# Optimization experiments

Measured on AMD Instinct MI355X. Metric: run time of the kernel, lower is better.

The kernel has to match this reference:

```python
import math
import jax, jax.numpy as jnp
import numpy as np

B = 4096
IN_FEATURES = 512
OUT_FEATURES = 1024
SPARSITY = 0.01  # kwta.sparsity
X_DENSITY = 0.1  # fraction of active bits in the binary SDR input


def setup_inputs() -> dict:
    key = jax.random.key(0)
    kx, kw = jax.random.split(key)
    # binary sparse SDR input (the module counts nonzeros, expects sparse binary x)
    x = (jax.random.uniform(kx, (B, IN_FEATURES)) < X_DENSITY).astype(jnp.float32)
    weight = jax.random.normal(kw, (OUT_FEATURES, IN_FEATURES), dtype=jnp.float32)
    return {"x": x, "weight": weight}


def reference(x, weight):
    Bn, in_f = x.shape
    out_f = weight.shape[0]
    k_active = math.ceil(SPARSITY * out_f)   # serial MP steps (11)
    k_in = math.ceil(SPARSITY * in_f)        # kwta winners on xr (6)
    rows = jnp.arange(Bn)

    nonzero = jnp.sum(x != 0, axis=1)
    lambd = (3 * jnp.max(nonzero) * in_f).astype(jnp.float32)

    def wta(r):  # one-hot argmax per row -> binary [B, out_f]
        idx = jnp.argmax(r, axis=1)
        return jnp.zeros_like(r).at[rows, idx].set(1.0)

    def kwta(v):  # binary top-k per row -> binary [B, in_f]
        _, idx = jax.lax.top_k(v, k_in)
        return jnp.zeros_like(v).at[rows[:, None], idx].set(1.0)

    two_x = 2.0 * x
    wT = weight.T  # [in_f, out_f]

    def step(carry, _):
        encoded, xr = carry
        residual = (two_x - xr) @ wT - lambd * encoded      # [B, out_f]
        encoded = encoded + wta(residual)
        xr = kwta(encoded @ weight)                          # [B, in_f]
        return (encoded, xr), None

    init = (jnp.zeros((Bn, out_f), jnp.float32), jnp.zeros_like(x))
    (encoded, xr), _ = jax.lax.scan(step, init, None, length=k_active)
    return encoded, xr
```

## Files before the change

kernel.cpp:

```cpp
#include <hip/hip_runtime.h>

#define IN_F 512
#define OUT_F 1024
#define K_ACTIVE 11
#define K_IN 6

__global__ __launch_bounds__(256) void transpose_w_kernel(const float* __restrict__ w,
                                                          float* __restrict__ wT) {
    __shared__ float tile[32][33];
    const int tx = threadIdx.x & 31;
    const int ty = threadIdx.x >> 5;
    const int i0 = blockIdx.x * 32;
    const int j0 = blockIdx.y * 32;
#pragma unroll
    for (int k = 0; k < 4; ++k)
        tile[ty + 8 * k][tx] = w[(size_t)(j0 + ty + 8 * k) * IN_F + (i0 + tx)];
    __syncthreads();
#pragma unroll
    for (int k = 0; k < 4; ++k)
        wT[(size_t)(i0 + ty + 8 * k) * OUT_F + (j0 + tx)] = tile[tx][ty + 8 * k];
}
__global__ void zero_row_f_kernel(float* __restrict__ wT) {
    wT[(size_t)IN_F * OUT_F + blockIdx.x * 256 + threadIdx.x] = 0.0f;
}

__device__ __forceinline__ unsigned long long pack_key(double v, unsigned rev,
                                                       unsigned long long mask) {
    unsigned long long b = (unsigned long long)__double_as_longlong(v);
    unsigned long long m =
        (unsigned long long)((long long)b >> 63) | 0x8000000000000000ull;
    unsigned long long u = b ^ m;
    return (u & ~mask) | (unsigned long long)rev;
}

__device__ __forceinline__ unsigned hi_key(double v) {
    const int hi = __double2hiint(v);
    return (unsigned)hi ^ ((unsigned)(hi >> 31) | 0x80000000u);
}

template <int C>
__device__ __forceinline__ unsigned maxdpp(unsigned v) {
    unsigned t = (unsigned)__builtin_amdgcn_update_dpp(0, (int)v, C, 0xF, 0xF, true);
    return t > v ? t : v;
}
__device__ __forceinline__ unsigned wave_umax(unsigned v) {
    v = maxdpp<0x111>(v);
    v = maxdpp<0x112>(v);
    v = maxdpp<0x114>(v);
    v = maxdpp<0x118>(v);
    v = maxdpp<0x142>(v);
    v = maxdpp<0x143>(v);
    return (unsigned)__builtin_amdgcn_readlane((int)v, 63);
}

__device__ __forceinline__ unsigned long long wave_max_key(unsigned long long k) {
    const unsigned h = (unsigned)(k >> 32), l = (unsigned)k;
    const unsigned gh = wave_umax(h);
    const unsigned long long tied = __ballot(h == gh);
    unsigned gl;
    if (__popcll(tied) == 1) {
        gl = (unsigned)__builtin_amdgcn_readlane((int)l,
                                                 (int)__ffsll((long long)tied) - 1);
    } else {
        gl = wave_umax((h == gh) ? l : 0u);
    }
    return ((unsigned long long)gh << 32) | gl;
}

__device__ __forceinline__ void half_add0(double* rh, const float* __restrict__ w,
                                          int i, int lane, int wv) {
#pragma unroll
    for (int s = 0; s < 8; ++s) {
        const int j = (wv << 9) | ((s >> 2) << 8) | (lane << 2) | (s & 3);
        rh[s] += (double)w[(size_t)j * IN_F + i];
    }
}
__device__ __forceinline__ void half_axpy0(double* rh, const float* __restrict__ w,
                                           int i, double sgn, int lane, int wv) {
#pragma unroll
    for (int s = 0; s < 8; ++s) {
        const int j = (wv << 9) | ((s >> 2) << 8) | (lane << 2) | (s & 3);
        rh[s] += sgn * (double)w[(size_t)j * IN_F + i];
    }
}

template <int MODE>
__global__ __launch_bounds__(128) void bmp_kernel(const float* __restrict__ x,
                                                  const float* __restrict__ w,
                                                  const float* __restrict__ wT,
                                                  float* __restrict__ out, int rows) {
    __shared__ unsigned short act[IN_F + 8];
    __shared__ unsigned gu32[2][2];
    __shared__ int gjw[2][2];
    __shared__ unsigned long long kx[2];
    __shared__ int axlist[16];
    __shared__ int axn;
    const int lane = threadIdx.x & 63;
    const int wv = threadIdx.x >> 6;
    const int row = blockIdx.x;
    if (row >= rows) return;

    const float* xrow = x + (size_t)row * IN_F;
    int cnt = 0;
#pragma unroll
    for (int c = 0; c < IN_F / 64; ++c) {
        bool pbit = xrow[c * 64 + lane] != 0.0f;
        unsigned long long m = __ballot(pbit);
        int pre = __popcll(m & ((1ull << lane) - 1ull));
        if (wv == 0 && pbit) act[cnt + pre] = (unsigned short)(c * 64 + lane);
        cnt += __popcll(m);
    }
    if (wv == 0 && lane < 2) act[cnt + lane] = (unsigned short)IN_F;
    __syncthreads();

    double r[8];
#pragma unroll
    for (int s = 0; s < 8; ++s) r[s] = 0.0;
    if constexpr (MODE == 1) {
        const int base = (wv << 9) + (lane << 2);
        const float* pa = wT + ((size_t)act[0] << 10) + base;
        const float* pb = wT + ((size_t)act[1] << 10) + base;
        float4 c0 = *(const float4*)pa, c1 = *(const float4*)(pa + 256);
        float4 c2 = *(const float4*)pb, c3 = *(const float4*)(pb + 256);
#pragma unroll 1
        for (int k = 0; k < cnt; k += 2) {
            float4 n0 = c0, n1 = c1, n2 = c2, n3 = c3;
            if (k + 2 < cnt) {
                const float* qa = wT + ((size_t)act[k + 2] << 10) + base;
                const float* qb = wT + ((size_t)act[k + 3] << 10) + base;
                n0 = *(const float4*)qa;  n1 = *(const float4*)(qa + 256);
                n2 = *(const float4*)qb;  n3 = *(const float4*)(qb + 256);
            }
            r[0] += (double)c0.x + (double)c2.x;  r[1] += (double)c0.y + (double)c2.y;
            r[2] += (double)c0.z + (double)c2.z;  r[3] += (double)c0.w + (double)c2.w;
            r[4] += (double)c1.x + (double)c3.x;  r[5] += (double)c1.y + (double)c3.y;
            r[6] += (double)c1.z + (double)c3.z;  r[7] += (double)c1.w + (double)c3.w;
            c0 = n0; c1 = n1; c2 = n2; c3 = n3;
        }
    } else {
#pragma unroll 1
        for (int k = 0; k < cnt; ++k) half_add0(r, w, act[k], lane, wv);
    }
#pragma unroll
    for (int s = 0; s < 8; ++s) r[s] *= 2.0;

    double vd[8];
#pragma unroll
    for (int p = 0; p < 8; ++p) vd[p] = 0.0;

    unsigned enc = 0;
    unsigned selmask = 0;
    int O0 = -1, O1 = -1, O2 = -1, O3 = -1, O4 = -1, O5 = -1;

#pragma unroll 1
    for (int t = 0; t < K_ACTIVE; ++t) {
        unsigned k8[8];
#pragma unroll
        for (int s = 0; s < 8; ++s) {
            const unsigned key = hi_key(r[s]);
            k8[s] = (enc & (1u << s)) ? 0u : key;
        }
        {
            unsigned lm = k8[0];
#pragma unroll
            for (int s = 1; s < 8; ++s) lm = k8[s] > lm ? k8[s] : lm;
            const unsigned g = wave_umax(lm);
            const unsigned long long tied = __ballot(lm == g);
            unsigned mm = 0;
#pragma unroll
            for (int s = 0; s < 8; ++s) mm |= (k8[s] == g) ? (1u << s) : 0u;
            const int L = (int)__ffsll((long long)tied) - 1;
            const unsigned mmL = (unsigned)__builtin_amdgcn_readlane((int)mm, L);
            int jw;
            if (__builtin_expect((__popcll(tied) == 1) && !(mmL & (mmL - 1)), 1)) {
                const int bi = __ffs(mmL) - 1;
                jw = (wv << 9) | ((bi >> 2) << 8) | (L << 2) | (bi & 3);
            } else {
                unsigned long long kb = 0;
#pragma unroll
                for (int s = 0; s < 8; ++s) {
                    const int j = (wv << 9) | ((s >> 2) << 8) | (lane << 2) | (s & 3);
                    const unsigned long long fk =
                        pack_key(r[s], 1023u ^ (unsigned)j, 1023ull);
                    kb = (k8[s] == g && fk > kb) ? fk : kb;
                }
                const unsigned long long gk = wave_max_key(kb);
                jw = 1023 ^ (int)(gk & 1023ull);
            }
            if (lane == 0) {
                gu32[t & 1][wv] = g;
                gjw[t & 1][wv] = jw;
            }
        }
        __syncthreads();
        const unsigned ga = gu32[t & 1][0], gb = gu32[t & 1][1];
        int bestj;
        if (__builtin_expect(ga != gb, 1)) {
            bestj = (gb > ga) ? gjw[t & 1][1] : gjw[t & 1][0];
        } else {
            unsigned long long kb = 0;
#pragma unroll
            for (int s = 0; s < 8; ++s) {
                const int j = (wv << 9) | ((s >> 2) << 8) | (lane << 2) | (s & 3);
                const unsigned long long fk =
                    pack_key(r[s], 1023u ^ (unsigned)j, 1023ull);
                kb = (k8[s] == ga && fk > kb) ? fk : kb;
            }
            const unsigned long long wm = wave_max_key(kb);
            if (lane == 0) kx[wv] = wm;
            __syncthreads();
            const unsigned long long A = kx[0], B = kx[1];
            bestj = 1023 ^ (int)((A > B ? A : B) & 1023ull);
        }
        bestj = __builtin_amdgcn_readfirstlane(bestj);
        if ((bestj >> 9) == wv && ((bestj >> 2) & 63) == lane)
            enc |= 1u << ((((bestj >> 8) & 1) << 2) | (bestj & 3));

        if (wv == 0) {
            const float* wr = w + ((size_t)bestj << 9) + (lane << 2);
            const float4 f0 = *(const float4*)wr;
            const float4 f1 = *(const float4*)(wr + 256);
            vd[0] += (double)f0.x;  vd[1] += (double)f0.y;
            vd[2] += (double)f0.z;  vd[3] += (double)f0.w;
            vd[4] += (double)f1.x;  vd[5] += (double)f1.y;
            vd[6] += (double)f1.z;  vd[7] += (double)f1.w;

            int N[6];
            unsigned kk[8];
#pragma unroll
            for (int p = 0; p < 8; ++p) kk[p] = hi_key(vd[p]);
#pragma unroll
            for (int s2 = 0; s2 < K_IN; ++s2) {
                unsigned lm = kk[0];
#pragma unroll
                for (int p = 1; p < 8; ++p) lm = kk[p] > lm ? kk[p] : lm;
                const unsigned g2 = wave_umax(lm);
                const unsigned long long tied2 = __ballot(lm == g2);
                unsigned mm2 = 0;
#pragma unroll
                for (int p = 0; p < 8; ++p) mm2 |= (kk[p] == g2) ? (1u << p) : 0u;
                const int L2 = (int)__ffsll((long long)tied2) - 1;
                const unsigned mmL2 =
                    (unsigned)__builtin_amdgcn_readlane((int)mm2, L2);
                int n;
                if (__builtin_expect((__popcll(tied2) == 1) && !(mmL2 & (mmL2 - 1)),
                                     1)) {
                    const int bp = __ffs(mmL2) - 1;
                    n = ((bp >> 2) << 8) | (L2 << 2) | (bp & 3);
#pragma unroll
                    for (int p = 0; p < 8; ++p) kk[p] = (kk[p] == g2) ? 0u : kk[p];
                } else {
                    unsigned long long kb = 0;
#pragma unroll
                    for (int p = 0; p < 8; ++p) {
                        const int i = ((p >> 2) << 8) | (lane << 2) | (p & 3);
                        const unsigned long long fk =
                            pack_key(vd[p], 511u ^ (unsigned)i, 511ull);
                        kb = (kk[p] == g2 && fk > kb) ? fk : kb;
                    }
                    const unsigned long long gk = wave_max_key(kb);
                    n = 511 ^ (int)(gk & 511ull);
                    const int ln = (n >> 2) & 63;
                    const int bp = (((n >> 8) & 1) << 2) | (n & 3);
#pragma unroll
                    for (int p = 0; p < 8; ++p)
                        kk[p] = (lane == ln && p == bp) ? 0u : kk[p];
                }
                N[s2] = __builtin_amdgcn_readfirstlane(n);
            }
            if (t == K_ACTIVE - 1) {
                selmask = 0;
#pragma unroll
                for (int p = 0; p < 8; ++p) selmask |= (kk[p] == 0u) ? (1u << p) : 0u;
            }

            if (lane == 0) {
                int n2 = 0;
                if (t == 0) {
#pragma unroll
                    for (int b = 0; b < 6; ++b) axlist[n2++] = ~N[b];
                } else if (t < K_ACTIVE - 1) {
#pragma unroll
                    for (int a2 = 0; a2 < 6; ++a2) {
                        const int o = (a2 == 0) ? O0 : (a2 == 1) ? O1 : (a2 == 2) ? O2
                                      : (a2 == 3) ? O3 : (a2 == 4) ? O4 : O5;
                        const bool stay = (o == N[0]) | (o == N[1]) | (o == N[2]) |
                                          (o == N[3]) | (o == N[4]) | (o == N[5]);
                        if (!stay) axlist[n2++] = o;
                    }
#pragma unroll
                    for (int b = 0; b < 6; ++b) {
                        const int nn = N[b];
                        const bool was = (nn == O0) | (nn == O1) | (nn == O2) |
                                         (nn == O3) | (nn == O4) | (nn == O5);
                        if (!was) axlist[n2++] = ~nn;
                    }
                }
                axn = n2;
            }
            O0 = N[0]; O1 = N[1]; O2 = N[2]; O3 = N[3]; O4 = N[4]; O5 = N[5];
        }
        __syncthreads();

        const int nax = axn;
        if (nax > 0) {
            if constexpr (MODE == 1) {
                const int base = (wv << 9) + (lane << 2);
                int e0 = axlist[0];
                {
                    const int i0 = (e0 < 0) ? ~e0 : e0;
                    const float* p = wT + ((size_t)i0 << 10) + base;
                    float4 A0 = *(const float4*)p;
                    float4 A1 = *(const float4*)(p + 256);
#pragma unroll 1
                    for (int k = 0; k < nax; ++k) {
                        float4 B0 = A0, B1 = A1;
                        int e1 = 0;
                        if (k + 1 < nax) {
                            e1 = axlist[k + 1];
                            const int i1 = (e1 < 0) ? ~e1 : e1;
                            const float* q = wT + ((size_t)i1 << 10) + base;
                            B0 = *(const float4*)q;
                            B1 = *(const float4*)(q + 256);
                        }
                        const double sg = (e0 < 0) ? -1.0 : 1.0;
                        r[0] += sg * (double)A0.x;  r[1] += sg * (double)A0.y;
                        r[2] += sg * (double)A0.z;  r[3] += sg * (double)A0.w;
                        r[4] += sg * (double)A1.x;  r[5] += sg * (double)A1.y;
                        r[6] += sg * (double)A1.z;  r[7] += sg * (double)A1.w;
                        A0 = B0; A1 = B1; e0 = e1;
                    }
                }
            } else {
#pragma unroll 1
                for (int k = 0; k < nax; ++k) {
                    const int e = axlist[k];
                    const int i = (e < 0) ? ~e : e;
                    half_axpy0(r, w, i, (e < 0) ? -1.0 : 1.0, lane, wv);
                }
            }
        }
    }

    float* oe = out + (size_t)row * OUT_F + (wv << 9) + (lane << 2);
#pragma unroll
    for (int c = 0; c < 2; ++c) {
        float4 v;
        v.x = (enc & (1u << (4 * c + 0))) ? 1.0f : 0.0f;
        v.y = (enc & (1u << (4 * c + 1))) ? 1.0f : 0.0f;
        v.z = (enc & (1u << (4 * c + 2))) ? 1.0f : 0.0f;
        v.w = (enc & (1u << (4 * c + 3))) ? 1.0f : 0.0f;
        *(float4*)(oe + (c << 8)) = v;
    }
    if (wv == 0) {
        float* ox = out + (size_t)rows * OUT_F + (size_t)row * IN_F + (lane << 2);
#pragma unroll
        for (int c = 0; c < 2; ++c) {
            float4 v;
            v.x = (selmask & (1u << (4 * c + 0))) ? 1.0f : 0.0f;
            v.y = (selmask & (1u << (4 * c + 1))) ? 1.0f : 0.0f;
            v.z = (selmask & (1u << (4 * c + 2))) ? 1.0f : 0.0f;
            v.w = (selmask & (1u << (4 * c + 3))) ? 1.0f : 0.0f;
            *(float4*)(ox + (c << 8)) = v;
        }
    }
}

extern "C" void kernel_launch(void* const* d_in, const int* in_sizes, int n_in,
                              void* d_out, int out_size, void* d_ws, size_t ws_size,
                              hipStream_t stream) {
    const float* x = (const float*)d_in[0];
    const float* w = (const float*)d_in[1];
    float* out = (float*)d_out;
    const int rows = in_sizes[0] / IN_F;

    const size_t need_f = (size_t)(IN_F + 1) * OUT_F * sizeof(float);

    if (d_ws != nullptr && ws_size >= need_f) {
        float* wT = (float*)d_ws;
        transpose_w_kernel<<<dim3(IN_F / 32, OUT_F / 32), 256, 0, stream>>>(w, wT);
        zero_row_f_kernel<<<OUT_F / 256, 256, 0, stream>>>(wT);
        bmp_kernel<1><<<rows, 128, 0, stream>>>(x, w, wT, out, rows);
    } else {
        bmp_kernel<0><<<rows, 128, 0, stream>>>(x, w, nullptr, out, rows);
    }
}
```

Baseline: 152.3 us.

## Process two rows per block, splitting serial kWTA work across waves

Each 128-thread block now handles two batch rows. Both waves share the argmax column scan for both rows, while each wave runs the serial encoded@W and top-k reconstruction for its own row, so that per-row serial work runs in parallel instead of leaving one wave idle. The aim is to remove idle wave time and halve the number of block-wide syncs per row. The cost is doubled register state (two residual vectors of doubles per thread) under a waves_per_eu hint, which may lower occupancy or cause spills.

```diff
diff --git a/kernel.cpp b/kernel.cpp
--- a/kernel.cpp
+++ b/kernel.cpp
@@ -85,118 +85,114 @@
 }
 
 template <int MODE>
-__global__ __launch_bounds__(128) void bmp_kernel(const float* __restrict__ x,
-                                                  const float* __restrict__ w,
-                                                  const float* __restrict__ wT,
-                                                  float* __restrict__ out, int rows) {
-    __shared__ unsigned short act[IN_F + 8];
+__global__ __attribute__((amdgpu_flat_work_group_size(128, 128),
+                          amdgpu_waves_per_eu(1, 4)))
+void bmp_kernel(const float* __restrict__ x, const float* __restrict__ w,
+                const float* __restrict__ wT, float* __restrict__ out, int rows) {
+    __shared__ unsigned short act[2][IN_F + 8];
+    __shared__ int cntS[2];
     __shared__ unsigned gu32[2][2];
     __shared__ int gjw[2][2];
-    __shared__ unsigned long long kx[2];
-    __shared__ int axlist[16];
-    __shared__ int axn;
+    __shared__ unsigned long long kx[2][2];
+    __shared__ int axlist[2][16];
+    __shared__ int axn[2];
     const int lane = threadIdx.x & 63;
     const int wv = threadIdx.x >> 6;
-    const int row = blockIdx.x;
-    if (row >= rows) return;
-
-    const float* xrow = x + (size_t)row * IN_F;
-    int cnt = 0;
-#pragma unroll
-    for (int c = 0; c < IN_F / 64; ++c) {
-        bool pbit = xrow[c * 64 + lane] != 0.0f;
-        unsigned long long m = __ballot(pbit);
-        int pre = __popcll(m & ((1ull << lane) - 1ull));
-        if (wv == 0 && pbit) act[cnt + pre] = (unsigned short)(c * 64 + lane);
-        cnt += __popcll(m);
-    }
-    if (wv == 0 && lane < 2) act[cnt + lane] = (unsigned short)IN_F;
+    const int rowA = blockIdx.x * 2;
+    if (rowA >= rows) return;
+    int rowB = rowA + 1;
+    if (rowB >= rows) rowB = rowA;
+    const int myrow = wv ? rowB : rowA;
+
+    {
+        const float* xrow = x + (size_t)myrow * IN_F;
+        int cnt = 0;
+#pragma unroll
+        for (int c = 0; c < IN_F / 64; ++c) {
+            bool pbit = xrow[c * 64 + lane] != 0.0f;
+            unsigned long long m = __ballot(pbit);
+            int pre = __popcll(m & ((1ull << lane) - 1ull));
+            if (pbit) act[wv][cnt + pre] = (unsigned short)(c * 64 + lane);
+            cnt += __popcll(m);
+        }
+        if (lane < 2) act[wv][cnt + lane] = (unsigned short)IN_F;
+        if (lane == 0) cntS[wv] = cnt;
+    }
     __syncthreads();
-
-    double r[8];
-#pragma unroll
-    for (int s = 0; s < 8; ++s) r[s] = 0.0;
+    const int cntA = cntS[0], cntB = cntS[1];
+
+    double rA[8], rB[8];
+#pragma unroll
+    for (int s = 0; s < 8; ++s) { rA[s] = 0.0; rB[s] = 0.0; }
+    const int base = (wv << 9) + (lane << 2);
     if constexpr (MODE == 1) {
-        const int base = (wv << 9) + (lane << 2);
-        const float* pa = wT + ((size_t)act[0] << 10) + base;
-        const float* pb = wT + ((size_t)act[1] << 10) + base;
-        float4 c0 = *(const float4*)pa, c1 = *(const float4*)(pa + 256);
-        float4 c2 = *(const float4*)pb, c3 = *(const float4*)(pb + 256);
-#pragma unroll 1
-        for (int k = 0; k < cnt; k += 2) {
-            float4 n0 = c0, n1 = c1, n2 = c2, n3 = c3;
-            if (k + 2 < cnt) {
-                const float* qa = wT + ((size_t)act[k + 2] << 10) + base;
-                const float* qb = wT + ((size_t)act[k + 3] << 10) + base;
-                n0 = *(const float4*)qa;  n1 = *(const float4*)(qa + 256);
-                n2 = *(const float4*)qb;  n3 = *(const float4*)(qb + 256);
-            }
-            r[0] += (double)c0.x + (double)c2.x;  r[1] += (double)c0.y + (double)c2.y;
-            r[2] += (double)c0.z + (double)c2.z;  r[3] += (double)c0.w + (double)c2.w;
-            r[4] += (double)c1.x + (double)c3.x;  r[5] += (double)c1.y + (double)c3.y;
-            r[6] += (double)c1.z + (double)c3.z;  r[7] += (double)c1.w + (double)c3.w;
-            c0 = n0; c1 = n1; c2 = n2; c3 = n3;
+#pragma unroll 1
+        for (int rl = 0; rl < 2; ++rl) {
+            double* r = rl ? rB : rA;
+            const unsigned short* a = act[rl];
+            const int cnt = rl ? cntB : cntA;
+            const float* pa = wT + ((size_t)a[0] << 10) + base;
+            const float* pb = wT + ((size_t)a[1] << 10) + base;
+            float4 c0 = *(const float4*)pa, c1 = *(const float4*)(pa + 256);
+            float4 c2 = *(const float4*)pb, c3 = *(const float4*)(pb + 256);
+#pragma unroll 1
+            for (int k = 0; k < cnt; k += 2) {
+                float4 n0 = c0, n1 = c1, n2 = c2, n3 = c3;
+                if (k + 2 < cnt) {
+                    const float* qa = wT + ((size_t)a[k + 2] << 10) + base;
+                    const float* qb = wT + ((size_t)a[k + 3] << 10) + base;
+                    n0 = *(const float4*)qa;  n1 = *(const float4*)(qa + 256);
+                    n2 = *(const float4*)qb;  n3 = *(const float4*)(qb + 256);
+                }
+                r[0] += (double)c0.x + (double)c2.x;
+                r[1] += (double)c0.y + (double)c2.y;
+                r[2] += (double)c0.z + (double)c2.z;
+                r[3] += (double)c0.w + (double)c2.w;
+                r[4] += (double)c1.x + (double)c3.x;
+                r[5] += (double)c1.y + (double)c3.y;
+                r[6] += (double)c1.z + (double)c3.z;
+                r[7] += (double)c1.w + (double)c3.w;
+                c0 = n0; c1 = n1; c2 = n2; c3 = n3;
+            }
         }
     } else {
 #pragma unroll 1
-        for (int k = 0; k < cnt; ++k) half_add0(r, w, act[k], lane, wv);
-    }
-#pragma unroll
-    for (int s = 0; s < 8; ++s) r[s] *= 2.0;
+        for (int k = 0; k < cntA; ++k) half_add0(rA, w, act[0][k], lane, wv);
+#pragma unroll 1
+        for (int k = 0; k < cntB; ++k) half_add0(rB, w, act[1][k], lane, wv);
+    }
+#pragma unroll
+    for (int s = 0; s < 8; ++s) { rA[s] *= 2.0; rB[s] *= 2.0; }
 
     double vd[8];
 #pragma unroll
     for (int p = 0; p < 8; ++p) vd[p] = 0.0;
 
-    unsigned enc = 0;
+    unsigned encA = 0, encB = 0;
     unsigned selmask = 0;
     int O0 = -1, O1 = -1, O2 = -1, O3 = -1, O4 = -1, O5 = -1;
 
-#pragma unroll 1
-    for (int t = 0; t < K_ACTIVE; ++t) {
+    auto amax_half = [&](const double* r, unsigned enc, int rsel) {
         unsigned k8[8];
 #pragma unroll
         for (int s = 0; s < 8; ++s) {
             const unsigned key = hi_key(r[s]);
             k8[s] = (enc & (1u << s)) ? 0u : key;
         }
-        {
-            unsigned lm = k8[0];
-#pragma unroll
-            for (int s = 1; s < 8; ++s) lm = k8[s] > lm ? k8[s] : lm;
-            const unsigned g = wave_umax(lm);
-            const unsigned long long tied = __ballot(lm == g);
-            unsigned mm = 0;
-#pragma unroll
-            for (int s = 0; s < 8; ++s) mm |= (k8[s] == g) ? (1u << s) : 0u;
-            const int L = (int)__ffsll((long long)tied) - 1;
-            const unsigned mmL = (unsigned)__builtin_amdgcn_readlane((int)mm, L);
-            int jw;
-            if (__builtin_expect((__popcll(tied) == 1) && !(mmL & (mmL - 1)), 1)) {
-                const int bi = __ffs(mmL) - 1;
-                jw = (wv << 9) | ((bi >> 2) << 8) | (L << 2) | (bi & 3);
-            } else {
-                unsigned long long kb = 0;
-#pragma unroll
-                for (int s = 0; s < 8; ++s) {
-                    const int j = (wv << 9) | ((s >> 2) << 8) | (lane << 2) | (s & 3);
-                    const unsigned long long fk =
-                        pack_key(r[s], 1023u ^ (unsigned)j, 1023ull);
-                    kb = (k8[s] == g && fk > kb) ? fk : kb;
-                }
-                const unsigned long long gk = wave_max_key(kb);
-                jw = 1023 ^ (int)(gk & 1023ull);
-            }
-            if (lane == 0) {
-                gu32[t & 1][wv] = g;
-                gjw[t & 1][wv] = jw;
-            }
-        }
-        __syncthreads();
-        const unsigned ga = gu32[t & 1][0], gb = gu32[t & 1][1];
-        int bestj;
-        if (__builtin_expect(ga != gb, 1)) {
-            bestj = (gb > ga) ? gjw[t & 1][1] : gjw[t & 1][0];
+        unsigned lm = k8[0];
+#pragma unroll
+        for (int s = 1; s < 8; ++s) lm = k8[s] > lm ? k8[s] : lm;
+        const unsigned g = wave_umax(lm);
+        const unsigned long long tied = __ballot(lm == g);
+        unsigned mm = 0;
+#pragma unroll
+        for (int s = 0; s < 8; ++s) mm |= (k8[s] == g) ? (1u << s) : 0u;
+        const int L = (int)__ffsll((long long)tied) - 1;
+        const unsigned mmL = (unsigned)__builtin_amdgcn_readlane((int)mm, L);
+        int jw;
+        if (__builtin_expect((__popcll(tied) == 1) && !(mmL & (mmL - 1)), 1)) {
+            const int bi = __ffs(mmL) - 1;
+            jw = (wv << 9) | ((bi >> 2) << 8) | (L << 2) | (bi & 3);
         } else {
             unsigned long long kb = 0;
 #pragma unroll
@@ -204,20 +200,56 @@
                 const int j = (wv << 9) | ((s >> 2) << 8) | (lane << 2) | (s & 3);
                 const unsigned long long fk =
                     pack_key(r[s], 1023u ^ (unsigned)j, 1023ull);
-                kb = (k8[s] == ga && fk > kb) ? fk : kb;
+                kb = (k8[s] == g && fk > kb) ? fk : kb;
+            }
+            const unsigned long long gk = wave_max_key(kb);
+            jw = 1023 ^ (int)(gk & 1023ull);
+        }
+        if (lane == 0) {
+            gu32[rsel][wv] = g;
+            gjw[rsel][wv] = jw;
+        }
+    };
+
+    auto merge_row = [&](int rsel, const double* r, unsigned enc) -> int {
+        const unsigned ga = gu32[rsel][0], gb = gu32[rsel][1];
+        int bestj;
+        if (__builtin_expect(ga != gb, 1)) {
+            bestj = (gb > ga) ? gjw[rsel][1] : gjw[rsel][0];
+        } else {
+            unsigned long long kb = 0;
+#pragma unroll
+            for (int s = 0; s < 8; ++s) {
+                const int j = (wv << 9) | ((s >> 2) << 8) | (lane << 2) | (s & 3);
+                const unsigned long long fk =
+                    pack_key(r[s], 1023u ^ (unsigned)j, 1023ull);
+                const bool cand = !(enc & (1u << s)) && hi_key(r[s]) == ga;
+                kb = (cand && fk > kb) ? fk : kb;
             }
             const unsigned long long wm = wave_max_key(kb);
-            if (lane == 0) kx[wv] = wm;
+            if (lane == 0) kx[rsel][wv] = wm;
             __syncthreads();
-            const unsigned long long A = kx[0], B = kx[1];
+            const unsigned long long A = kx[rsel][0], B = kx[rsel][1];
             bestj = 1023 ^ (int)((A > B ? A : B) & 1023ull);
         }
-        bestj = __builtin_amdgcn_readfirstlane(bestj);
-        if ((bestj >> 9) == wv && ((bestj >> 2) & 63) == lane)
-            enc |= 1u << ((((bestj >> 8) & 1) << 2) | (bestj & 3));
-
-        if (wv == 0) {
-            const float* wr = w + ((size_t)bestj << 9) + (lane << 2);
+        return __builtin_amdgcn_readfirstlane(bestj);
+    };
+
+#pragma unroll 1
+    for (int t = 0; t < K_ACTIVE; ++t) {
+        amax_half(rA, encA, 0);
+        amax_half(rB, encB, 1);
+        __syncthreads();
+        const int bestjA = merge_row(0, rA, encA);
+        const int bestjB = merge_row(1, rB, encB);
+        if ((bestjA >> 9) == wv && ((bestjA >> 2) & 63) == lane)
+            encA |= 1u << ((((bestjA >> 8) & 1) << 2) | (bestjA & 3));
+        if ((bestjB >> 9) == wv && ((bestjB >> 2) & 63) == lane)
+            encB |= 1u << ((((bestjB >> 8) & 1) << 2) | (bestjB & 3));
+
+        {
+            const int bj = wv ? bestjB : bestjA;
+            const float* wr = w + ((size_t)bj << 9) + (lane << 2);
             const float4 f0 = *(const float4*)wr;
             const float4 f1 = *(const float4*)(wr + 256);
             vd[0] += (double)f0.x;  vd[1] += (double)f0.y;
@@ -278,7 +310,7 @@
                 int n2 = 0;
                 if (t == 0) {
 #pragma unroll
-                    for (int b = 0; b < 6; ++b) axlist[n2++] = ~N[b];
+                    for (int b = 0; b < 6; ++b) axlist[wv][n2++] = ~N[b];
                 } else if (t < K_ACTIVE - 1) {
 #pragma unroll
                     for (int a2 = 0; a2 < 6; ++a2) {
@@ -286,28 +318,29 @@
                                       : (a2 == 3) ? O3 : (a2 == 4) ? O4 : O5;
                         const bool stay = (o == N[0]) | (o == N[1]) | (o == N[2]) |
                                           (o == N[3]) | (o == N[4]) | (o == N[5]);
-                        if (!stay) axlist[n2++] = o;
+                        if (!stay) axlist[wv][n2++] = o;
                     }
 #pragma unroll
                     for (int b = 0; b < 6; ++b) {
                         const int nn = N[b];
                         const bool was = (nn == O0) | (nn == O1) | (nn == O2) |
                                          (nn == O3) | (nn == O4) | (nn == O5);
-                        if (!was) axlist[n2++] = ~nn;
+                        if (!was) axlist[wv][n2++] = ~nn;
                     }
                 }
-                axn = n2;
+                axn[wv] = n2;
             }
             O0 = N[0]; O1 = N[1]; O2 = N[2]; O3 = N[3]; O4 = N[4]; O5 = N[5];
         }
         __syncthreads();
 
-        const int nax = axn;
-        if (nax > 0) {
-            if constexpr (MODE == 1) {
-                const int base = (wv << 9) + (lane << 2);
-                int e0 = axlist[0];
-                {
+#pragma unroll
+        for (int rl = 0; rl < 2; ++rl) {
+            double* r = rl ? rB : rA;
+            const int nax = axn[rl];
+            if (nax > 0) {
+                if constexpr (MODE == 1) {
+                    int e0 = axlist[rl][0];
                     const int i0 = (e0 < 0) ? ~e0 : e0;
                     const float* p = wT + ((size_t)i0 << 10) + base;
                     float4 A0 = *(const float4*)p;
@@ -317,7 +350,7 @@
                         float4 B0 = A0, B1 = A1;
                         int e1 = 0;
                         if (k + 1 < nax) {
-                            e1 = axlist[k + 1];
+                            e1 = axlist[rl][k + 1];
                             const int i1 = (e1 < 0) ? ~e1 : e1;
                             const float* q = wT + ((size_t)i1 << 10) + base;
                             B0 = *(const float4*)q;
@@ -330,30 +363,40 @@
                         r[6] += sg * (double)A1.z;  r[7] += sg * (double)A1.w;
                         A0 = B0; A1 = B1; e0 = e1;
                     }
+                } else {
+#pragma unroll 1
+                    for (int k = 0; k < nax; ++k) {
+                        const int e = axlist[rl][k];
+                        const int i = (e < 0) ? ~e : e;
+                        half_axpy0(r, w, i, (e < 0) ? -1.0 : 1.0, lane, wv);
+                    }
                 }
-            } else {
-#pragma unroll 1
-                for (int k = 0; k < nax; ++k) {
-                    const int e = axlist[k];
-                    const int i = (e < 0) ? ~e : e;
-                    half_axpy0(r, w, i, (e < 0) ? -1.0 : 1.0, lane, wv);
-                }
-            }
-        }
-    }
-
-    float* oe = out + (size_t)row * OUT_F + (wv << 9) + (lane << 2);
-#pragma unroll
-    for (int c = 0; c < 2; ++c) {
-        float4 v;
-        v.x = (enc & (1u << (4 * c + 0))) ? 1.0f : 0.0f;
-        v.y = (enc & (1u << (4 * c + 1))) ? 1.0f : 0.0f;
-        v.z = (enc & (1u << (4 * c + 2))) ? 1.0f : 0.0f;
-        v.w = (enc & (1u << (4 * c + 3))) ? 1.0f : 0.0f;
-        *(float4*)(oe + (c << 8)) = v;
-    }
-    if (wv == 0) {
-        float* ox = out + (size_t)rows * OUT_F + (size_t)row * IN_F + (lane << 2);
+            }
+        }
+    }
+
+    {
+        float* oeA = out + (size_t)rowA * OUT_F + (wv << 9) + (lane << 2);
+#pragma unroll
+        for (int c = 0; c < 2; ++c) {
+            float4 v;
+            v.x = (encA & (1u << (4 * c + 0))) ? 1.0f : 0.0f;
+            v.y = (encA & (1u << (4 * c + 1))) ? 1.0f : 0.0f;
+            v.z = (encA & (1u << (4 * c + 2))) ? 1.0f : 0.0f;
+            v.w = (encA & (1u << (4 * c + 3))) ? 1.0f : 0.0f;
+            *(float4*)(oeA + (c << 8)) = v;
+        }
+        float* oeB = out + (size_t)rowB * OUT_F + (wv << 9) + (lane << 2);
+#pragma unroll
+        for (int c = 0; c < 2; ++c) {
+            float4 v;
+            v.x = (encB & (1u << (4 * c + 0))) ? 1.0f : 0.0f;
+            v.y = (encB & (1u << (4 * c + 1))) ? 1.0f : 0.0f;
+            v.z = (encB & (1u << (4 * c + 2))) ? 1.0f : 0.0f;
+            v.w = (encB & (1u << (4 * c + 3))) ? 1.0f : 0.0f;
+            *(float4*)(oeB + (c << 8)) = v;
+        }
+        float* ox = out + (size_t)rows * OUT_F + (size_t)myrow * IN_F + (lane << 2);
 #pragma unroll
         for (int c = 0; c < 2; ++c) {
             float4 v;
@@ -375,13 +418,14 @@
     const int rows = in_sizes[0] / IN_F;
 
     const size_t need_f = (size_t)(IN_F + 1) * OUT_F * sizeof(float);
+    const int blocks = (rows + 1) / 2;
 
     if (d_ws != nullptr && ws_size >= need_f) {
         float* wT = (float*)d_ws;
         transpose_w_kernel<<<dim3(IN_F / 32, OUT_F / 32), 256, 0, stream>>>(w, wT);
         zero_row_f_kernel<<<OUT_F / 256, 256, 0, stream>>>(wT);
-        bmp_kernel<1><<<rows, 128, 0, stream>>>(x, w, wT, out, rows);
+        bmp_kernel<1><<<blocks, 128, 0, stream>>>(x, w, wT, out, rows);
     } else {
-        bmp_kernel<0><<<rows, 128, 0, stream>>>(x, w, nullptr, out, rows);
-    }
-}
+        bmp_kernel<0><<<blocks, 128, 0, stream>>>(x, w, nullptr, out, rows);
+    }
+}
```

New measurement: 177.2 us. 16.3% more time.
